# Kernel optimization log

Hardware: AMD Instinct MI355X
Metric: run time of the kernel (lower is better)

The kernel has to match this reference:

```python
import jax, jax.numpy as jnp
import numpy as np

B, C, H, W = 4, 64, 128, 128
CO, K, PAD, STRIDE = 64, 3, 1, 1


def setup_inputs() -> dict:
    key = jax.random.key(0)
    k1, k2, k3 = jax.random.split(key, 3)
    x = jax.random.normal(k1, (B, C, H, W), dtype=jnp.float32)
    # small offset weights so predicted offsets stay near the regular grid
    w_off = jax.random.normal(k2, (2 * K * K, C, K, K), dtype=jnp.float32) * 0.01
    b_off = jnp.zeros((2 * K * K,), dtype=jnp.float32)
    w_def = jax.random.normal(k3, (CO, C, K, K), dtype=jnp.float32) * (1.0 / np.sqrt(C * K * K))
    return {"x": x, "w_off": w_off, "b_off": b_off, "w_def": w_def}


def _deform_forward(x, w_off, b_off, w_def):
    Bs, Cs, Hs, Ws = x.shape
    Co = w_def.shape[0]
    KK = K * K
    # offset conv: [B, 2*K*K, Ho, Wo]
    off = jax.lax.conv_general_dilated(
        x, w_off, (STRIDE, STRIDE), [(PAD, PAD), (PAD, PAD)],
        dimension_numbers=("NCHW", "OIHW", "NCHW"))
    off = off + b_off[None, :, None, None]
    Ho, Wo = off.shape[2], off.shape[3]
    off = off.reshape(Bs, KK, 2, Ho, Wo)  # channel 2k -> dy, 2k+1 -> dx
    ky = (jnp.arange(KK) // K).astype(x.dtype)
    kx = (jnp.arange(KK) % K).astype(x.dtype)
    gy = (jnp.arange(Ho) * STRIDE - PAD).astype(x.dtype)
    gx = (jnp.arange(Wo) * STRIDE - PAD).astype(x.dtype)
    # sampling positions per (batch, tap, out_y, out_x)
    py = off[:, :, 0] + ky[None, :, None, None] + gy[None, None, :, None]
    px = off[:, :, 1] + kx[None, :, None, None] + gx[None, None, None, :]
    y0 = jnp.floor(py)
    x0 = jnp.floor(px)
    dy = py - y0
    dx = px - x0
    y0i = y0.astype(jnp.int32)
    x0i = x0.astype(jnp.int32)
    xf = x.reshape(Bs, Cs, Hs * Ws)

    def gather(iy, ix):
        valid = (iy >= 0) & (iy < Hs) & (ix >= 0) & (ix < Ws)
        idx = jnp.clip(iy, 0, Hs - 1) * Ws + jnp.clip(ix, 0, Ws - 1)  # [B,KK,Ho,Wo]
        g = jax.vmap(lambda xb, ib: jnp.take(xb, ib.reshape(-1), axis=1))(xf, idx)
        g = g.reshape(Bs, Cs, KK, Ho, Wo)
        return g * valid[:, None].astype(x.dtype)

    # bilinear sample with zero padding outside the image (torchvision semantics)
    sampled = gather(y0i, x0i) * ((1 - dy) * (1 - dx))[:, None]
    sampled = sampled + gather(y0i, x0i + 1) * ((1 - dy) * dx)[:, None]
    sampled = sampled + gather(y0i + 1, x0i) * (dy * (1 - dx))[:, None]
    sampled = sampled + gather(y0i + 1, x0i + 1) * (dy * dx)[:, None]
    # conv-style weighted accumulation over (channel, tap)
    return jnp.einsum("bckhw,ock->bohw", sampled, w_def.reshape(Co, Cs, KK))


def reference(x, w_off, b_off, w_def):
    return _deform_forward(x, w_off, b_off, w_def)
```

## Files before the change

### kernel.cpp

```cpp
#include <hip/hip_runtime.h>
#include <math.h>


typedef short  v4s __attribute__((ext_vector_type(4)));
typedef short  v8s __attribute__((ext_vector_type(8)));
typedef float  v4f __attribute__((ext_vector_type(4)));

namespace {
constexpr int Bn = 4, Cn = 64, Hn = 128, Wn = 128, COn = 64;
constexpr int HWn = 16384;
constexpr int CKn = 576;
constexpr int TILE = 16;
constexpr int RS = 580;
constexpr size_t XT_OFF   = 0;
constexpr size_t ASWZ_OFF = (size_t)Bn * HWn * Cn;
constexpr size_t AOFF_OFF = ASWZ_OFF + 18432;
}

__device__ __forceinline__ unsigned short f2bf(float f) {
    union { float f; unsigned int u; } v; v.f = f;
    unsigned int u = v.u;
    u += 0x7fffu + ((u >> 16) & 1u);
    return (unsigned short)(u >> 16);
}
__device__ __forceinline__ unsigned int pack2bf(float a, float b) {
    return (unsigned int)f2bf(a) | ((unsigned int)f2bf(b) << 16);
}

__global__ __launch_bounds__(256) void k_transpose(const float* __restrict__ x,
                                                   float* __restrict__ xt) {
    __shared__ float tile[64][65];
    const int tid  = threadIdx.x;
    const int lane = tid & 63;
    const int grp  = tid >> 6;
    const int b    = blockIdx.x >> 8;
    const int hw0  = (blockIdx.x & 255) << 6;
#pragma unroll
    for (int r = 0; r < 16; ++r) {
        const int c = (r << 2) + grp;
        tile[c][lane] = x[(b * Cn + c) * HWn + hw0 + lane];
    }
    __syncthreads();
#pragma unroll
    for (int r = 0; r < 16; ++r) {
        const int hwl = (r << 2) + grp;
        xt[(size_t)(b * HWn + hw0 + hwl) * Cn + lane] = tile[lane][hwl];
    }
}

__global__ __launch_bounds__(256) void k_prep(const float* __restrict__ w_def,
                                              const float* __restrict__ w_off,
                                              unsigned short* __restrict__ aswz,
                                              unsigned short* __restrict__ aoff) {
    const int idx = blockIdx.x * 256 + threadIdx.x;
    if (idx < 36864) {
        const int j = idx & 7;
        const int l = (idx >> 3) & 63;
        const int s = (idx >> 9) % 18;
        const int r = idx / 9216;
        const int co = 16 * r + (l & 15);
        const int kk = 32 * s + 4 * (l >> 4) + (j & 3) + 16 * (j >> 2);
        const int tap = kk >> 6, c = kk & 63;
        aswz[idx] = f2bf(w_def[co * CKn + c * 9 + tap]);
    } else {
        const int i2 = idx - 36864;
        const int j = i2 & 7;
        const int l = (i2 >> 3) & 63;
        const int s = (i2 >> 9) % 18;
        const int r = i2 / 9216;
        const int co = 16 * r + (l & 15);
        const int kk = 32 * s + 4 * (l >> 4) + (j & 3) + 16 * (j >> 2);
        const int tap = kk >> 6, c = kk & 63;
        aoff[i2] = (co < 18) ? f2bf(w_off[co * CKn + c * 9 + tap]) : (unsigned short)0;
    }
}

__global__ __launch_bounds__(256, 6) void k_deform(const float* __restrict__ xt,
                                                   const unsigned short* __restrict__ aoff,
                                                   const float* __restrict__ b_off,
                                                   const unsigned short* __restrict__ aswz,
                                                   float* __restrict__ out) {
    __shared__ unsigned short Bl[TILE * RS];
    __shared__ float part[4][18][16];
    __shared__ float offl[18][16];
    uint2* Bl2 = (uint2*)Bl;
    const int tid  = threadIdx.x;
    const int lane = tid & 63;
    const int wid  = tid >> 6;
    const int g    = lane >> 4;
    const int c15  = lane & 15;
    const int q    = lane & 15;
    const int pq   = lane >> 4;
    const int b    = blockIdx.x >> 10;
    const int p0   = (blockIdx.x & 1023) * TILE;
    const int pix  = (wid << 2) + pq;
    const int p    = p0 + pix;
    const int oy   = p >> 7;
    const int ox   = p & (Wn - 1);
    const float* xc = xt + (size_t)(b * HWn) * Cn + 4 * q;

#pragma unroll
    for (int k = 0; k < 9; ++k) {
        const int sy = oy + k / 3 - 1;
        const int sx = ox + k % 3 - 1;
        float4 t = {0.f, 0.f, 0.f, 0.f};
        if ((unsigned)sy < (unsigned)Hn && (unsigned)sx < (unsigned)Wn)
            t = *reinterpret_cast<const float4*>(xc + (size_t)(sy * Wn + sx) * Cn);
        Bl2[pix * 145 + k * 16 + q] = make_uint2(pack2bf(t.x, t.y), pack2bf(t.z, t.w));
    }
    __syncthreads();

    {
        v4f pa00 = {0.f,0.f,0.f,0.f};
        v4f pa10 = {0.f,0.f,0.f,0.f};
        for (int s = wid; s < 18; s += 4) {
            const int kb = 32 * s + 4 * g;
            const unsigned short* b0p = &Bl[c15 * RS + kb];
            const v4s lo0 = *reinterpret_cast<const v4s*>(b0p);
            const v4s hi0 = *reinterpret_cast<const v4s*>(b0p + 16);
            const v8s bb0 = {lo0[0],lo0[1],lo0[2],lo0[3],hi0[0],hi0[1],hi0[2],hi0[3]};
            const v8s a0 = *reinterpret_cast<const v8s*>(aoff + (size_t)(0 * 18 + s) * 512 + lane * 8);
            const v8s a1 = *reinterpret_cast<const v8s*>(aoff + (size_t)(1 * 18 + s) * 512 + lane * 8);
            pa00 = __builtin_amdgcn_mfma_f32_16x16x32_bf16(a0, bb0, pa00, 0, 0, 0);
            pa10 = __builtin_amdgcn_mfma_f32_16x16x32_bf16(a1, bb0, pa10, 0, 0, 0);
        }
#pragma unroll
        for (int r = 0; r < 4; ++r) {
            const int co0 = (g << 2) + r;
            part[wid][co0][c15] = pa00[r];
            const int co1 = 16 + (g << 2) + r;
            if (co1 < 18)
                part[wid][co1][c15] = pa10[r];
        }
    }
    __syncthreads();
    for (int idx = tid; idx < 288; idx += 256) {
        const int ch = idx >> 4, px = idx & 15;
        offl[ch][px] = part[0][ch][px] + part[1][ch][px] + part[2][ch][px]
                     + part[3][ch][px] + b_off[ch];
    }
    __syncthreads();

#pragma unroll
    for (int k = 0; k < 9; ++k) {
        const float py = offl[2 * k][pix]     + (float)(oy + k / 3 - 1);
        const float px = offl[2 * k + 1][pix] + (float)(ox + k % 3 - 1);
        const float fy = floorf(py);
        const float fx = floorf(px);
        const float ay = py - fy;
        const float ax = px - fx;
        const int iy0 = (int)fy;
        const int ix0 = (int)fx;
        const float w00 = (1.f - ay) * (1.f - ax);
        const float w01 = (1.f - ay) * ax;
        const float w10 = ay * (1.f - ax);
        const float w11 = ay * ax;
        float4 v = {0.f, 0.f, 0.f, 0.f};
        const bool x0ok = (unsigned)ix0 < (unsigned)Wn;
        const bool x1ok = (unsigned)(ix0 + 1) < (unsigned)Wn;
        const float* r0 = xc + (ptrdiff_t)iy0 * (Wn * Cn);
        if ((unsigned)iy0 < (unsigned)Hn) {
            if (x0ok) { const float4 t = *reinterpret_cast<const float4*>(r0 + ix0 * Cn);
                        v.x = fmaf(w00, t.x, v.x); v.y = fmaf(w00, t.y, v.y);
                        v.z = fmaf(w00, t.z, v.z); v.w = fmaf(w00, t.w, v.w); }
            if (x1ok) { const float4 t = *reinterpret_cast<const float4*>(r0 + ix0 * Cn + Cn);
                        v.x = fmaf(w01, t.x, v.x); v.y = fmaf(w01, t.y, v.y);
                        v.z = fmaf(w01, t.z, v.z); v.w = fmaf(w01, t.w, v.w); }
        }
        if ((unsigned)(iy0 + 1) < (unsigned)Hn) {
            const float* r1 = r0 + Wn * Cn;
            if (x0ok) { const float4 t = *reinterpret_cast<const float4*>(r1 + ix0 * Cn);
                        v.x = fmaf(w10, t.x, v.x); v.y = fmaf(w10, t.y, v.y);
                        v.z = fmaf(w10, t.z, v.z); v.w = fmaf(w10, t.w, v.w); }
            if (x1ok) { const float4 t = *reinterpret_cast<const float4*>(r1 + ix0 * Cn + Cn);
                        v.x = fmaf(w11, t.x, v.x); v.y = fmaf(w11, t.y, v.y);
                        v.z = fmaf(w11, t.z, v.z); v.w = fmaf(w11, t.w, v.w); }
        }
        Bl2[pix * 145 + k * 16 + q] = make_uint2(pack2bf(v.x, v.y), pack2bf(v.z, v.w));
    }
    __syncthreads();

    v4f acc0 = {0.f,0.f,0.f,0.f};
    const unsigned short* arow = aswz + (size_t)wid * 9216 + lane * 8;
#pragma unroll
    for (int s = 0; s < 18; ++s) {
        const v8s a = *reinterpret_cast<const v8s*>(arow + s * 512);
        const int kb = 32 * s + 4 * g;
        const unsigned short* b0p = &Bl[c15 * RS + kb];
        const v4s lo0 = *reinterpret_cast<const v4s*>(b0p);
        const v4s hi0 = *reinterpret_cast<const v4s*>(b0p + 16);
        const v8s bb0 = {lo0[0],lo0[1],lo0[2],lo0[3],hi0[0],hi0[1],hi0[2],hi0[3]};
        acc0 = __builtin_amdgcn_mfma_f32_16x16x32_bf16(a, bb0, acc0, 0, 0, 0);
    }
    const int co = (wid << 4) + (g << 2);
    float* op = out + ((size_t)(b * COn + co)) * HWn + p0 + c15;
#pragma unroll
    for (int r = 0; r < 4; ++r)
        op[(size_t)r * HWn] = acc0[r];
}

extern "C" void kernel_launch(void* const* d_in, const int* in_sizes, int n_in,
                              void* d_out, int out_size, void* d_ws, size_t ws_size,
                              hipStream_t stream) {
    const float* x     = (const float*)d_in[0];
    const float* w_off = (const float*)d_in[1];
    const float* b_off = (const float*)d_in[2];
    const float* w_def = (const float*)d_in[3];
    float* outp = (float*)d_out;
    float* wsf  = (float*)d_ws;
    float* xt   = wsf + XT_OFF;
    unsigned short* aswz = (unsigned short*)(wsf + ASWZ_OFF);
    unsigned short* aoff = (unsigned short*)(wsf + AOFF_OFF);

    k_transpose<<<Bn * 256, 256, 0, stream>>>(x, xt);
    k_prep<<<216, 256, 0, stream>>>(w_def, w_off, aswz, aoff);
    k_deform<<<Bn * (HWn / TILE), 256, 0, stream>>>(xt, aoff, b_off, aswz, outp);
}
```

Measured before the change: 65.71 us.

## Store input as zero-padded bf16 NHWC halo buffer to drop bounds checks

The transpose kernel now writes the input as bf16 pairs into a channel-last buffer with a 2-pixel zero halo, cleared each call by a memset. The deform kernel then loads neighbours and bilinear taps without per-tap bounds branches, clamping sample coordinates into the halo instead. This halves gather bytes and removes divergent branches. In exchange it adds a memset pass and rounds the input to bf16 before interpolation rather than after.

```diff
diff --git a/kernel.cpp b/kernel.cpp
--- a/kernel.cpp
+++ b/kernel.cpp
@@ -5,6 +5,7 @@
 typedef short  v4s __attribute__((ext_vector_type(4)));
 typedef short  v8s __attribute__((ext_vector_type(8)));
 typedef float  v4f __attribute__((ext_vector_type(4)));
+typedef float  v2f __attribute__((ext_vector_type(2)));
 
 namespace {
 constexpr int Bn = 4, Cn = 64, Hn = 128, Wn = 128, COn = 64;
@@ -12,8 +13,10 @@
 constexpr int CKn = 576;
 constexpr int TILE = 16;
 constexpr int RS = 580;
-constexpr size_t XT_OFF   = 0;
-constexpr size_t ASWZ_OFF = (size_t)Bn * HWn * Cn;
+constexpr int HW2 = 132;
+constexpr int XPITCH = HW2 * 16;
+constexpr size_t XH_OFF   = 0;
+constexpr size_t ASWZ_OFF = 2230272;
 constexpr size_t AOFF_OFF = ASWZ_OFF + 18432;
 }
 
@@ -26,9 +29,15 @@
 __device__ __forceinline__ unsigned int pack2bf(float a, float b) {
     return (unsigned int)f2bf(a) | ((unsigned int)f2bf(b) << 16);
 }
-
-__global__ __launch_bounds__(256) void k_transpose(const float* __restrict__ x,
-                                                   float* __restrict__ xt) {
+__device__ __forceinline__ v2f unpk(unsigned int u) {
+    v2f r;
+    r.x = __uint_as_float(u << 16);
+    r.y = __uint_as_float(u & 0xffff0000u);
+    return r;
+}
+
+__global__ __launch_bounds__(256) void k_halo(const float* __restrict__ x,
+                                              unsigned int* __restrict__ xh) {
     __shared__ float tile[64][65];
     const int tid  = threadIdx.x;
     const int lane = tid & 63;
@@ -41,10 +50,16 @@
         tile[c][lane] = x[(b * Cn + c) * HWn + hw0 + lane];
     }
     __syncthreads();
-#pragma unroll
-    for (int r = 0; r < 16; ++r) {
-        const int hwl = (r << 2) + grp;
-        xt[(size_t)(b * HWn + hw0 + hwl) * Cn + lane] = tile[lane][hwl];
+    const int h = lane >> 5;
+    const int m = lane & 31;
+#pragma unroll
+    for (int r = 0; r < 8; ++r) {
+        const int hwl = (r << 3) + (grp << 1) + h;
+        const int hw  = hw0 + hwl;
+        const int yy  = hw >> 7;
+        const int xx  = hw & (Wn - 1);
+        const unsigned int u = pack2bf(tile[2 * m][hwl], tile[2 * m + 1][hwl]);
+        xh[((size_t)(b * HW2 + yy + 2) * HW2 + (xx + 2)) * 32 + m] = u;
     }
 }
 
@@ -75,7 +90,7 @@
     }
 }
 
-__global__ __launch_bounds__(256, 6) void k_deform(const float* __restrict__ xt,
+__global__ __launch_bounds__(256, 6) void k_deform(const uint2* __restrict__ xh2,
                                                    const unsigned short* __restrict__ aoff,
                                                    const float* __restrict__ b_off,
                                                    const unsigned short* __restrict__ aswz,
@@ -97,16 +112,14 @@
     const int p    = p0 + pix;
     const int oy   = p >> 7;
     const int ox   = p & (Wn - 1);
-    const float* xc = xt + (size_t)(b * HWn) * Cn + 4 * q;
+    const int xbase = b * (HW2 * HW2 * 16);
 
 #pragma unroll
     for (int k = 0; k < 9; ++k) {
         const int sy = oy + k / 3 - 1;
         const int sx = ox + k % 3 - 1;
-        float4 t = {0.f, 0.f, 0.f, 0.f};
-        if ((unsigned)sy < (unsigned)Hn && (unsigned)sx < (unsigned)Wn)
-            t = *reinterpret_cast<const float4*>(xc + (size_t)(sy * Wn + sx) * Cn);
-        Bl2[pix * 145 + k * 16 + q] = make_uint2(pack2bf(t.x, t.y), pack2bf(t.z, t.w));
+        const uint2 t = xh2[xbase + ((sy + 2) * HW2 + (sx + 2)) * 16 + q];
+        Bl2[pix * 145 + k * 16 + q] = t;
     }
     __syncthreads();
 
@@ -149,34 +162,28 @@
         const float fx = floorf(px);
         const float ay = py - fy;
         const float ax = px - fx;
-        const int iy0 = (int)fy;
-        const int ix0 = (int)fx;
+        int iy0 = (int)fy;
+        int ix0 = (int)fx;
+        iy0 = max(-2, min(iy0, 128));
+        ix0 = max(-2, min(ix0, 128));
         const float w00 = (1.f - ay) * (1.f - ax);
         const float w01 = (1.f - ay) * ax;
         const float w10 = ay * (1.f - ax);
         const float w11 = ay * ax;
-        float4 v = {0.f, 0.f, 0.f, 0.f};
-        const bool x0ok = (unsigned)ix0 < (unsigned)Wn;
-        const bool x1ok = (unsigned)(ix0 + 1) < (unsigned)Wn;
-        const float* r0 = xc + (ptrdiff_t)iy0 * (Wn * Cn);
-        if ((unsigned)iy0 < (unsigned)Hn) {
-            if (x0ok) { const float4 t = *reinterpret_cast<const float4*>(r0 + ix0 * Cn);
-                        v.x = fmaf(w00, t.x, v.x); v.y = fmaf(w00, t.y, v.y);
-                        v.z = fmaf(w00, t.z, v.z); v.w = fmaf(w00, t.w, v.w); }
-            if (x1ok) { const float4 t = *reinterpret_cast<const float4*>(r0 + ix0 * Cn + Cn);
-                        v.x = fmaf(w01, t.x, v.x); v.y = fmaf(w01, t.y, v.y);
-                        v.z = fmaf(w01, t.z, v.z); v.w = fmaf(w01, t.w, v.w); }
-        }
-        if ((unsigned)(iy0 + 1) < (unsigned)Hn) {
-            const float* r1 = r0 + Wn * Cn;
-            if (x0ok) { const float4 t = *reinterpret_cast<const float4*>(r1 + ix0 * Cn);
-                        v.x = fmaf(w10, t.x, v.x); v.y = fmaf(w10, t.y, v.y);
-                        v.z = fmaf(w10, t.z, v.z); v.w = fmaf(w10, t.w, v.w); }
-            if (x1ok) { const float4 t = *reinterpret_cast<const float4*>(r1 + ix0 * Cn + Cn);
-                        v.x = fmaf(w11, t.x, v.x); v.y = fmaf(w11, t.y, v.y);
-                        v.z = fmaf(w11, t.z, v.z); v.w = fmaf(w11, t.w, v.w); }
-        }
-        Bl2[pix * 145 + k * 16 + q] = make_uint2(pack2bf(v.x, v.y), pack2bf(v.z, v.w));
+        const uint2* r0 = xh2 + xbase + ((iy0 + 2) * HW2 + (ix0 + 2)) * 16 + q;
+        const uint2 u00 = r0[0];
+        const uint2 u01 = r0[16];
+        const uint2 u10 = r0[XPITCH];
+        const uint2 u11 = r0[XPITCH + 16];
+        v2f va = unpk(u00.x) * w00;
+        va += unpk(u01.x) * w01;
+        va += unpk(u10.x) * w10;
+        va += unpk(u11.x) * w11;
+        v2f vb = unpk(u00.y) * w00;
+        vb += unpk(u01.y) * w01;
+        vb += unpk(u10.y) * w10;
+        vb += unpk(u11.y) * w11;
+        Bl2[pix * 145 + k * 16 + q] = make_uint2(pack2bf(va.x, va.y), pack2bf(vb.x, vb.y));
     }
     __syncthreads();
 
@@ -208,11 +215,12 @@
     const float* w_def = (const float*)d_in[3];
     float* outp = (float*)d_out;
     float* wsf  = (float*)d_ws;
-    float* xt   = wsf + XT_OFF;
+    unsigned int* xh = (unsigned int*)(wsf + XH_OFF);
     unsigned short* aswz = (unsigned short*)(wsf + ASWZ_OFF);
     unsigned short* aoff = (unsigned short*)(wsf + AOFF_OFF);
 
-    k_transpose<<<Bn * 256, 256, 0, stream>>>(x, xt);
+    hipMemsetAsync(xh, 0, (size_t)Bn * HW2 * HW2 * Cn * 2, stream);
+    k_halo<<<Bn * 256, 256, 0, stream>>>(x, xh);
     k_prep<<<216, 256, 0, stream>>>(w_def, w_off, aswz, aoff);
-    k_deform<<<Bn * (HWn / TILE), 256, 0, stream>>>(xt, aoff, b_off, aswz, outp);
-}
+    k_deform<<<Bn * (HWn / TILE), 256, 0, stream>>>((const uint2*)xh, aoff, b_off, aswz, outp);
+}
```

Result: faster. 56.21 us (-14.5%).
